# Optimization experiments

Hardware: AMD Instinct MI355X
Metric: run time of the kernel (lower is better)

## Reference

```python
import jax, jax.numpy as jnp
import numpy as np

D_MODEL = 768
D_STATE = 16
D_CONV = 4
EXPAND = 2
HEADDIM = 64
D_INNER = EXPAND * D_MODEL          # 1536
NHEADS = D_INNER // HEADDIM         # 24
CONV_DIM = D_INNER + 2 * D_STATE    # 1568
D_IN_PROJ = 2 * D_INNER + 2 * D_STATE + NHEADS  # 3128
BATCH, SEQ = 4, 2048


def _mamba_params(key, scale=0.02):
    ks = jax.random.split(key, 5)
    return dict(
        in_w=jax.random.normal(ks[0], (D_MODEL, D_IN_PROJ), jnp.float32) * scale,
        conv_w=jax.random.normal(ks[1], (CONV_DIM, D_CONV), jnp.float32) * scale,
        conv_b=jnp.zeros((CONV_DIM,), jnp.float32),
        dt_bias=jax.random.normal(ks[2], (NHEADS,), jnp.float32) * 0.1,
        A_log=jnp.log(jax.random.uniform(ks[3], (NHEADS,), jnp.float32, 1.0, 16.0)),
        D=jnp.ones((NHEADS,), jnp.float32),
        norm_w=jnp.ones((D_INNER,), jnp.float32),
        out_w=jax.random.normal(ks[4], (D_INNER, D_MODEL), jnp.float32) * scale,
    )


def setup_inputs() -> dict:
    key = jax.random.key(0)
    kx, kf, kb, k1, k2 = jax.random.split(key, 5)
    f = _mamba_params(kf)
    b = _mamba_params(kb)
    k1a, k1b = jax.random.split(k1)
    inp = {
        'x': jax.random.normal(kx, (BATCH, SEQ, D_MODEL), jnp.float32),
        'ln1_w': jnp.ones((D_MODEL,), jnp.float32), 'ln1_b': jnp.zeros((D_MODEL,), jnp.float32),
        'ln2_w': jnp.ones((D_MODEL,), jnp.float32), 'ln2_b': jnp.zeros((D_MODEL,), jnp.float32),
        'ffn_w1': jax.random.normal(k1a, (2 * D_MODEL, 4 * D_MODEL), jnp.float32) * 0.02,
        'ffn_b1': jnp.zeros((4 * D_MODEL,), jnp.float32),
        'ffn_w2': jax.random.normal(k1b, (4 * D_MODEL, D_MODEL), jnp.float32) * 0.02,
        'ffn_b2': jnp.zeros((D_MODEL,), jnp.float32),
    }
    for name, p in (('f', f), ('b', b)):
        for k, v in p.items():
            inp[name + '_' + k] = v
    return inp


def _layernorm(x, w, b, eps=1e-5):
    m = jnp.mean(x, -1, keepdims=True)
    v = jnp.mean((x - m) ** 2, -1, keepdims=True)
    return (x - m) * jax.lax.rsqrt(v + eps) * w + b


def _mamba2(u, in_w, conv_w, conv_b, dt_bias, A_log, D, norm_w, out_w):
    b, l, _ = u.shape
    zxbcdt = u @ in_w                               # (b,l,d_in_proj)
    z = zxbcdt[..., :D_INNER]
    xBC = zxbcdt[..., D_INNER:D_INNER + CONV_DIM]
    dt = jax.nn.softplus(zxbcdt[..., -NHEADS:] + dt_bias)   # (b,l,h)
    # depthwise causal conv1d (kernel D_CONV) + SiLU
    xpad = jnp.pad(xBC, ((0, 0), (D_CONV - 1, 0), (0, 0)))
    xc = sum(conv_w[:, k] * xpad[:, k:k + l, :] for k in range(D_CONV)) + conv_b
    xc = jax.nn.silu(xc)
    xh = xc[..., :D_INNER].reshape(b, l, NHEADS, HEADDIM)
    Bm = xc[..., D_INNER:D_INNER + D_STATE]          # (b,l,n), ngroups=1
    Cm = xc[..., D_INNER + D_STATE:]                 # (b,l,n)
    A = -jnp.exp(A_log)                              # (h,)
    dA = jnp.exp(dt * A)                             # (b,l,h)

    def step(h, inp):
        dA_t, dt_t, B_t, C_t, x_t = inp              # (b,h),(b,h),(b,n),(b,n),(b,h,p)
        h = h * dA_t[:, :, None, None] + (dt_t[:, :, None] * x_t)[..., None] * B_t[:, None, None, :]
        y = jnp.einsum('bhpn,bn->bhp', h, C_t)
        return h, y

    h0 = jnp.zeros((b, NHEADS, HEADDIM, D_STATE), u.dtype)
    xs = (dA.transpose(1, 0, 2), dt.transpose(1, 0, 2), Bm.transpose(1, 0, 2),
          Cm.transpose(1, 0, 2), xh.transpose(1, 0, 2, 3))
    _, ys = jax.lax.scan(step, h0, xs)               # ys: (l,b,h,p)
    y = ys.transpose(1, 0, 2, 3) + D[None, None, :, None] * xh
    y = y.reshape(b, l, D_INNER)
    # gated RMSNorm: rmsnorm(y * silu(z)) * weight
    yz = y * jax.nn.silu(z)
    yz = yz * jax.lax.rsqrt(jnp.mean(yz * yz, -1, keepdims=True) + 1e-5) * norm_w
    return yz @ out_w


def reference(x, ln1_w, ln1_b, ln2_w, ln2_b,
              f_in_w, f_conv_w, f_conv_b, f_dt_bias, f_A_log, f_D, f_norm_w, f_out_w,
              b_in_w, b_conv_w, b_conv_b, b_dt_bias, b_A_log, b_D, b_norm_w, b_out_w,
              ffn_w1, ffn_b1, ffn_w2, ffn_b2):
    xn = _layernorm(x, ln1_w, ln1_b)
    fo = _mamba2(xn, f_in_w, f_conv_w, f_conv_b, f_dt_bias, f_A_log, f_D, f_norm_w, f_out_w)
    bo = _mamba2(jnp.flip(xn, 1), b_in_w, b_conv_w, b_conv_b, b_dt_bias, b_A_log, b_D, b_norm_w, b_out_w)
    bo = jnp.flip(bo, 1)
    bi = jnp.concatenate([fo, bo], -1)
    h = jax.nn.gelu(bi @ ffn_w1 + ffn_b1, approximate=False)
    h = jax.nn.gelu(h @ ffn_w2 + ffn_b2, approximate=False)
    # dropout is identity in eval mode
    return _layernorm(x + h, ln2_w, ln2_b)
```

## Files before the change

kernel.cpp:

```cpp
#include <hip/hip_runtime.h>
#include <math.h>

#define BATCH   4
#define SEQ     2048
#define DMODEL  768
#define DSTATE  16
#define DCONV   4
#define HEADDIM 64
#define DINNER  1536
#define NHEADS  24
#define CONVDIM 1568
#define DINPROJ 3128
#define DFFN    3072
#define ROWS    (BATCH*SEQ)
#define QCH     128
#define NCHUNK  (SEQ/QCH)

typedef __attribute__((ext_vector_type(8))) short bhalf8;
typedef __attribute__((ext_vector_type(4))) float floatx4;

__device__ __forceinline__ float gelu_f(float x) {
    return 0.5f * x * (1.0f + erff(x * 0.70710678118654752f));
}

__device__ __forceinline__ void splitRNE(float v, unsigned short& h, unsigned short& l) {
    unsigned u = __float_as_uint(v);
    unsigned rr = u + 0x7FFFu + ((u >> 16) & 1u);
    unsigned short hi = (unsigned short)(rr >> 16);
    float rem = v - __uint_as_float(((unsigned)hi) << 16);
    unsigned u2 = __float_as_uint(rem);
    unsigned r2 = u2 + 0x7FFFu + ((u2 >> 16) & 1u);
    h = hi;
    l = (unsigned short)(r2 >> 16);
}

__device__ __forceinline__ void gl16(const unsigned short* g, unsigned short* l) {
    __builtin_amdgcn_global_load_lds(
        (const __attribute__((address_space(1))) void*)g,
        (__attribute__((address_space(3))) void*)l, 16, 0, 0);
}

__device__ __forceinline__ void bar() {
    asm volatile("" ::: "memory");
    __builtin_amdgcn_s_barrier();
    asm volatile("" ::: "memory");
}

__device__ __forceinline__ float2 blockReduce2(float a, float b) {
    #pragma unroll
    for (int o = 32; o > 0; o >>= 1) {
        a += __shfl_down(a, o, 64);
        b += __shfl_down(b, o, 64);
    }
    __shared__ float sa[4], sb[4];
    int w = threadIdx.x >> 6, lane = threadIdx.x & 63;
    if (lane == 0) { sa[w] = a; sb[w] = b; }
    __syncthreads();
    if (threadIdx.x == 0) {
        int nw = blockDim.x >> 6;
        for (int i = 1; i < nw; ++i) { a += sa[i]; b += sb[i]; }
        sa[0] = a; sb[0] = b;
    }
    __syncthreads();
    return make_float2(sa[0], sb[0]);
}

__global__ __launch_bounds__(256) void ln_kernel(
    const float* __restrict__ x, const float* __restrict__ res,
    const float* __restrict__ w, const float* __restrict__ b,
    float* __restrict__ out)
{
    int r = blockIdx.x;
    const float* xr = x + (size_t)r * DMODEL;
    float v[3]; float s = 0.f, ss = 0.f;
    #pragma unroll
    for (int i = 0; i < 3; ++i) {
        int c = threadIdx.x + i * 256;
        float t = xr[c];
        if (res) t += res[(size_t)r * DMODEL + c];
        v[i] = t; s += t; ss += t * t;
    }
    float2 red = blockReduce2(s, ss);
    float mean = red.x * (1.0f / DMODEL);
    float var  = red.y * (1.0f / DMODEL) - mean * mean;
    float inv  = rsqrtf(var + 1e-5f);
    #pragma unroll
    for (int i = 0; i < 3; ++i) {
        int c = threadIdx.x + i * 256;
        out[(size_t)r * DMODEL + c] = (v[i] - mean) * inv * w[c] + b[c];
    }
}

__global__ __launch_bounds__(256) void ln_split_kernel(
    const float* __restrict__ x,
    const float* __restrict__ w, const float* __restrict__ b,
    unsigned short* __restrict__ H, unsigned short* __restrict__ L)
{
    int r = blockIdx.x;
    const float* xr = x + (size_t)r * DMODEL;
    float v[3]; float s = 0.f, ss = 0.f;
    #pragma unroll
    for (int i = 0; i < 3; ++i) {
        int c = threadIdx.x + i * 256;
        float t = xr[c];
        v[i] = t; s += t; ss += t * t;
    }
    float2 red = blockReduce2(s, ss);
    float mean = red.x * (1.0f / DMODEL);
    float var  = red.y * (1.0f / DMODEL) - mean * mean;
    float inv  = rsqrtf(var + 1e-5f);
    #pragma unroll
    for (int i = 0; i < 3; ++i) {
        int c = threadIdx.x + i * 256;
        float o = (v[i] - mean) * inv * w[c] + b[c];
        unsigned short h, l;
        splitRNE(o, h, l);
        H[(size_t)r * DMODEL + c] = h;
        L[(size_t)r * DMODEL + c] = l;
    }
}

__global__ __launch_bounds__(256) void wconv(
    const float* __restrict__ W, unsigned short* __restrict__ TH,
    unsigned short* __restrict__ TL, int K, int N)
{
    __shared__ float t[32][33];
    int tx = threadIdx.x & 31, ty = threadIdx.x >> 5;
    int kb = blockIdx.y * 32, nb = blockIdx.x * 32;
    #pragma unroll
    for (int i = 0; i < 4; ++i) {
        int k = kb + ty + i * 8, n = nb + tx;
        t[ty + i * 8][tx] = (k < K && n < N) ? W[(size_t)k * N + n] : 0.f;
    }
    __syncthreads();
    #pragma unroll
    for (int i = 0; i < 4; ++i) {
        int n = nb + ty + i * 8, k = kb + tx;
        if (n < N && k < K) {
            unsigned short hi, lo;
            splitRNE(t[tx][ty + i * 8], hi, lo);
            TH[(size_t)n * K + k] = hi;
            TL[(size_t)n * K + k] = lo;
        }
    }
}

__global__ __launch_bounds__(256) void gemm3(
    const unsigned short* __restrict__ AHg, const unsigned short* __restrict__ ALg,
    const unsigned short* __restrict__ BHg, const unsigned short* __restrict__ BLg,
    float* __restrict__ C, unsigned short* __restrict__ CHo, unsigned short* __restrict__ CLo,
    const float* __restrict__ bias,
    int M, int N, int K, int ldc, int coloff,
    int revA, int revC, int act)
{
    (void)M;
    __shared__ __align__(16) unsigned short AsH[2][128 * 32], AsL[2][128 * 32];
    __shared__ __align__(16) unsigned short BsH[2][128 * 32], BsL[2][128 * 32];

    const int tid = threadIdx.x;
    const int m0 = blockIdx.y * 128;
    const int n0 = blockIdx.x * 128;

    size_t aoff[2], boff[2];
    int lofs[2];
    #pragma unroll
    for (int q = 0; q < 2; ++q) {
        int row = (tid >> 2) + 64 * q;
        int sd  = (tid & 3) ^ ((row >> 1) & 3);
        int ar = m0 + row;
        if (revA) ar = (ar & ~(SEQ - 1)) + (SEQ - 1 - (ar & (SEQ - 1)));
        aoff[q] = (size_t)ar * K + sd * 8;
        boff[q] = (size_t)(n0 + row) * K + sd * 8;
        lofs[q] = (tid + 256 * q) * 8;
    }

    auto stage = [&](int k0, int b) {
        #pragma unroll
        for (int q = 0; q < 2; ++q) {
            gl16(AHg + aoff[q] + k0, &AsH[b][lofs[q]]);
            gl16(ALg + aoff[q] + k0, &AsL[b][lofs[q]]);
            gl16(BHg + boff[q] + k0, &BsH[b][lofs[q]]);
            gl16(BLg + boff[q] + k0, &BsL[b][lofs[q]]);
        }
    };

    auto frag = [&](const unsigned short* buf, int row, int slot) -> bhalf8 {
        int sp = slot ^ ((row >> 1) & 3);
        return *(const bhalf8*)(buf + row * 32 + sp * 8);
    };

    const int w = tid >> 6, lane = tid & 63;
    const int rw = (w >> 1) * 64, cw = (w & 1) * 64;
    const int lr = lane & 15;
    const int lq = lane >> 4;

    floatx4 acc[4][4];
    const floatx4 fz = {0.f, 0.f, 0.f, 0.f};
    #pragma unroll
    for (int i = 0; i < 4; ++i)
        #pragma unroll
        for (int j = 0; j < 4; ++j) acc[i][j] = fz;

    const int ktiles = K >> 5;
    stage(0, 0);
    asm volatile("s_waitcnt vmcnt(0)" ::: "memory");
    bar();

    for (int kt = 0; kt < ktiles; ++kt) {
        const int cb = kt & 1;
        if (kt + 1 < ktiles) stage((kt + 1) * 32, cb ^ 1);

        const unsigned short* pAH = AsH[cb];
        const unsigned short* pAL = AsL[cb];
        const unsigned short* pBH = BsH[cb];
        const unsigned short* pBL = BsL[cb];
        bhalf8 ah[4], al[4], bh[4], bl[4];
        #pragma unroll
        for (int i = 0; i < 4; ++i) {
            int ra = rw + i * 16 + lr;
            int rb = cw + i * 16 + lr;
            ah[i] = frag(pAH, ra, lq);
            al[i] = frag(pAL, ra, lq);
            bh[i] = frag(pBH, rb, lq);
            bl[i] = frag(pBL, rb, lq);
        }

        __builtin_amdgcn_s_setprio(1);
        #pragma unroll
        for (int i = 0; i < 4; ++i)
            #pragma unroll
            for (int j = 0; j < 4; ++j) {
                acc[i][j] = __builtin_amdgcn_mfma_f32_16x16x32_bf16(ah[i], bh[j], acc[i][j], 0, 0, 0);
                acc[i][j] = __builtin_amdgcn_mfma_f32_16x16x32_bf16(ah[i], bl[j], acc[i][j], 0, 0, 0);
                acc[i][j] = __builtin_amdgcn_mfma_f32_16x16x32_bf16(al[i], bh[j], acc[i][j], 0, 0, 0);
            }
        __builtin_amdgcn_s_setprio(0);

        asm volatile("s_waitcnt vmcnt(0)" ::: "memory");
        bar();
    }

    #pragma unroll
    for (int i = 0; i < 4; ++i) {
        #pragma unroll
        for (int j = 0; j < 4; ++j) {
            int gc = n0 + cw + j * 16 + lr;
            if (gc < N) {
                float bv = bias ? bias[gc] : 0.f;
                #pragma unroll
                for (int rg = 0; rg < 4; ++rg) {
                    int gm = m0 + rw + i * 16 + lq * 4 + rg;
                    if (revC) gm = (gm & ~(SEQ - 1)) + (SEQ - 1 - (gm & (SEQ - 1)));
                    float v = acc[i][j][rg] + bv;
                    if (act) v = gelu_f(v);
                    size_t o = (size_t)gm * ldc + coloff + gc;
                    if (CHo) {
                        unsigned short h, l;
                        splitRNE(v, h, l);
                        CHo[o] = h; CLo[o] = l;
                    } else {
                        C[o] = v;
                    }
                }
            }
        }
    }
}

__global__ __launch_bounds__(256) void conv_kernel(
    const float* __restrict__ zx, const float* __restrict__ cw,
    const float* __restrict__ cb, float* __restrict__ xcv,
    float* __restrict__ bc)
{
    int cg = blockIdx.x * 256 + threadIdx.x;
    if (cg >= CONVDIM / 4) return;
    int c = cg * 4;
    int r = blockIdx.y;
    int t = r & (SEQ - 1);
    int rb = r & ~(SEQ - 1);
    float4 acc = *(const float4*)&cb[c];
    #pragma unroll
    for (int k = 0; k < DCONV; ++k) {
        int tt = t - (DCONV - 1) + k;
        if (tt >= 0) {
            float4 xv = *(const float4*)&zx[(size_t)(rb + tt) * DINPROJ + DINNER + c];
            acc.x += cw[(c + 0) * DCONV + k] * xv.x;
            acc.y += cw[(c + 1) * DCONV + k] * xv.y;
            acc.z += cw[(c + 2) * DCONV + k] * xv.z;
            acc.w += cw[(c + 3) * DCONV + k] * xv.w;
        }
    }
    float4 v;
    v.x = acc.x / (1.0f + expf(-acc.x));
    v.y = acc.y / (1.0f + expf(-acc.y));
    v.z = acc.z / (1.0f + expf(-acc.z));
    v.w = acc.w / (1.0f + expf(-acc.w));
    if (c < DINNER) *(float4*)&xcv[(size_t)r * DINNER + c] = v;
    else            *(float4*)&bc[(size_t)r * 32 + (c - DINNER)] = v;
}

__global__ __launch_bounds__(256) void dt_kernel(
    const float* __restrict__ zx, const float* __restrict__ dt_bias,
    const float* __restrict__ A_log, float* __restrict__ dtda)
{
    int i = blockIdx.x * 256 + threadIdx.x;
    if (i >= ROWS * NHEADS) return;
    int r = i / NHEADS, h = i - r * NHEADS;
    float v = zx[(size_t)r * DINPROJ + (DINPROJ - NHEADS) + h] + dt_bias[h];
    float dt = (v > 20.f) ? v : log1pf(expf(v));
    float A = -expf(A_log[h]);
    float2 o = make_float2(dt, expf(dt * A));
    *(float2*)&dtda[(size_t)r * 48 + 2 * h] = o;
}

__global__ __launch_bounds__(64) void scan_a(
    const float* __restrict__ xcv, const float* __restrict__ bc,
    const float* __restrict__ dtda, const float* __restrict__ Dp,
    float* __restrict__ yout, float* __restrict__ S, float* __restrict__ cd)
{
    int blk = blockIdx.x;
    int bh = blk / NCHUNK, c = blk - bh * NCHUNK;
    int b = bh / NHEADS, h = bh - b * NHEADS;
    int p = threadIdx.x;
    float hs[DSTATE] = {};
    float Dv = Dp[h];
    float cum = 1.f;
    int t0 = c * QCH;
    for (int t = t0; t < t0 + QCH; ++t) {
        size_t r = (size_t)b * SEQ + t;
        float2 dd = *(const float2*)&dtda[r * 48 + 2 * h];
        float dt = dd.x;
        float dA = dd.y;
        float x  = xcv[r * DINNER + h * HEADDIM + p];
        cum *= dA;
        float coef = dt * x;
        const float* bcr = bc + r * 32;
        float y = 0.f;
        #pragma unroll
        for (int n = 0; n < DSTATE; ++n) {
            hs[n] = hs[n] * dA + coef * bcr[n];
            y += hs[n] * bcr[16 + n];
        }
        yout[r * DINPROJ + DINNER + h * HEADDIM + p] = y + Dv * x;
        if (p == 0) cd[r * NHEADS + h] = cum;
    }
    float* Sp = S + (((size_t)bh * NCHUNK + c) * HEADDIM + p) * DSTATE;
    #pragma unroll
    for (int n = 0; n < DSTATE; ++n) Sp[n] = hs[n];
}

__global__ __launch_bounds__(64) void scan_b(
    const float* __restrict__ cd, float* __restrict__ S)
{
    int bh = blockIdx.x;
    int b = bh / NHEADS, h = bh - b * NHEADS;
    int p = threadIdx.x;
    float H[DSTATE] = {};
    for (int c = 0; c < NCHUNK; ++c) {
        float* Sp = S + (((size_t)bh * NCHUNK + c) * HEADDIM + p) * DSTATE;
        float P = cd[((size_t)b * SEQ + c * QCH + QCH - 1) * NHEADS + h];
        float s[DSTATE];
        #pragma unroll
        for (int n = 0; n < DSTATE; ++n) s[n] = Sp[n];
        #pragma unroll
        for (int n = 0; n < DSTATE; ++n) Sp[n] = H[n];
        #pragma unroll
        for (int n = 0; n < DSTATE; ++n) H[n] = P * H[n] + s[n];
    }
}

__global__ __launch_bounds__(64) void scan_c(
    const float* __restrict__ bc, const float* __restrict__ cd,
    const float* __restrict__ S, float* __restrict__ yout)
{
    int blk = blockIdx.x;
    int bh = blk / (NCHUNK - 1), c = blk - bh * (NCHUNK - 1) + 1;
    int b = bh / NHEADS, h = bh - b * NHEADS;
    int p = threadIdx.x;
    const float* Hp = S + (((size_t)bh * NCHUNK + c) * HEADDIM + p) * DSTATE;
    float H[DSTATE];
    #pragma unroll
    for (int n = 0; n < DSTATE; ++n) H[n] = Hp[n];
    int t0 = c * QCH;
    for (int t = t0; t < t0 + QCH; ++t) {
        size_t r = (size_t)b * SEQ + t;
        const float* Cr = bc + r * 32 + 16;
        float dot = 0.f;
        #pragma unroll
        for (int n = 0; n < DSTATE; ++n) dot += H[n] * Cr[n];
        float cum = cd[r * NHEADS + h];
        yout[r * DINPROJ + DINNER + h * HEADDIM + p] += cum * dot;
    }
}

__global__ __launch_bounds__(256) void gnorm_kernel(
    const float* __restrict__ zx, const float* __restrict__ nw,
    unsigned short* __restrict__ H, unsigned short* __restrict__ L)
{
    int r = blockIdx.x;
    const float* zr = zx + (size_t)r * DINPROJ;
    float v[6]; float ss = 0.f;
    #pragma unroll
    for (int i = 0; i < 6; ++i) {
        int c = threadIdx.x + i * 256;
        float z = zr[c];
        float y = zr[DINNER + c];
        float t = y * z / (1.0f + expf(-z));
        v[i] = t; ss += t * t;
    }
    float2 red = blockReduce2(ss, 0.f);
    float sc = rsqrtf(red.x * (1.0f / DINNER) + 1e-5f);
    #pragma unroll
    for (int i = 0; i < 6; ++i) {
        int c = threadIdx.x + i * 256;
        float o = v[i] * sc * nw[c];
        unsigned short h, l;
        splitRNE(o, h, l);
        H[(size_t)r * DINNER + c] = h;
        L[(size_t)r * DINNER + c] = l;
    }
}

extern "C" void kernel_launch(void* const* d_in, const int* in_sizes, int n_in,
                              void* d_out, int out_size, void* d_ws, size_t ws_size,
                              hipStream_t stream)
{
    (void)in_sizes; (void)n_in; (void)out_size; (void)ws_size;
    const float* x     = (const float*)d_in[0];
    const float* ln1w  = (const float*)d_in[1];
    const float* ln1b  = (const float*)d_in[2];
    const float* ln2w  = (const float*)d_in[3];
    const float* ln2b  = (const float*)d_in[4];
    const float* ffnw1 = (const float*)d_in[5];
    const float* ffnb1 = (const float*)d_in[6];
    const float* ffnw2 = (const float*)d_in[7];
    const float* ffnb2 = (const float*)d_in[8];
    const float* p[2][8];
    for (int d = 0; d < 2; ++d)
        for (int i = 0; i < 8; ++i)
            p[d][i] = (const float*)d_in[9 + d * 8 + i];

    float* ws   = (float*)d_ws;
    float* zx   = ws;
    float* bi   = zx + (size_t)ROWS * DINPROJ;
    float* S    = bi + (size_t)ROWS * DINNER;
    float* Wbuf = S  + (size_t)ROWS * DINNER;
    float* bcb  = Wbuf + 2402304;
    float* dtda = bcb + (size_t)ROWS * 32;
    float* Sbuf = Wbuf;
    float* cdbf = Wbuf + (size_t)BATCH * NHEADS * NCHUNK * HEADDIM * DSTATE;

    unsigned short* xnH = (unsigned short*)d_out;
    unsigned short* xnL = xnH + (size_t)ROWS * DMODEL;
    float* xcv = S;
    unsigned short* znH = (unsigned short*)S;
    unsigned short* znL = znH + (size_t)ROWS * DINNER;
    unsigned short* biH = (unsigned short*)bi;
    unsigned short* biL = biH + (size_t)ROWS * DINNER;
    unsigned short* hmH = (unsigned short*)zx;
    unsigned short* hmL = hmH + (size_t)ROWS * DFFN;
    float* ffo = S + 4718592;

    ln_split_kernel<<<ROWS, 256, 0, stream>>>(x, ln1w, ln1b, xnH, xnL);

    for (int d = 0; d < 2; ++d) {
        unsigned short* WH = (unsigned short*)Wbuf;
        unsigned short* WL = WH + (size_t)DINPROJ * DMODEL;
        wconv<<<dim3((DINPROJ + 31) / 32, DMODEL / 32), 256, 0, stream>>>(
            p[d][0], WH, WL, DMODEL, DINPROJ);
        gemm3<<<dim3((DINPROJ + 127) / 128, ROWS / 128), 256, 0, stream>>>(
            xnH, xnL, WH, WL, zx, nullptr, nullptr, nullptr,
            ROWS, DINPROJ, DMODEL, DINPROJ, 0, d, 0, 0);
        conv_kernel<<<dim3(2, ROWS), 256, 0, stream>>>(zx, p[d][1], p[d][2], xcv, bcb);
        dt_kernel<<<(ROWS * NHEADS + 255) / 256, 256, 0, stream>>>(
            zx, p[d][3], p[d][4], dtda);
        scan_a<<<BATCH * NHEADS * NCHUNK, 64, 0, stream>>>(
            xcv, bcb, dtda, p[d][5], zx, Sbuf, cdbf);
        scan_b<<<BATCH * NHEADS, 64, 0, stream>>>(cdbf, Sbuf);
        scan_c<<<BATCH * NHEADS * (NCHUNK - 1), 64, 0, stream>>>(
            bcb, cdbf, Sbuf, zx);
        gnorm_kernel<<<ROWS, 256, 0, stream>>>(zx, p[d][6], znH, znL);
        unsigned short* WL2 = WH + (size_t)DMODEL * DINNER;
        wconv<<<dim3(DMODEL / 32, DINNER / 32), 256, 0, stream>>>(
            p[d][7], WH, WL2, DINNER, DMODEL);
        gemm3<<<dim3(DMODEL / 128, ROWS / 128), 256, 0, stream>>>(
            znH, znL, WH, WL2, nullptr, biH, biL, nullptr,
            ROWS, DMODEL, DINNER, DINNER, d * DMODEL, 0, d, 0);
    }

    {
        unsigned short* WH = (unsigned short*)S;
        unsigned short* WL = WH + (size_t)DFFN * DINNER;
        wconv<<<dim3(DFFN / 32, DINNER / 32), 256, 0, stream>>>(
            ffnw1, WH, WL, DINNER, DFFN);
        gemm3<<<dim3(DFFN / 128, ROWS / 128), 256, 0, stream>>>(
            biH, biL, WH, WL, nullptr, hmH, hmL, ffnb1,
            ROWS, DFFN, DINNER, DFFN, 0, 0, 0, 1);
    }
    {
        unsigned short* WH = (unsigned short*)S;
        unsigned short* WL = WH + (size_t)DMODEL * DFFN;
        wconv<<<dim3(DMODEL / 32, DFFN / 32), 256, 0, stream>>>(
            ffnw2, WH, WL, DFFN, DMODEL);
        gemm3<<<dim3(DMODEL / 128, ROWS / 128), 256, 0, stream>>>(
            hmH, hmL, WH, WL, ffo, nullptr, nullptr, ffnb2,
            ROWS, DMODEL, DFFN, DMODEL, 0, 0, 0, 1);
    }
    ln_kernel<<<ROWS, 256, 0, stream>>>(x, ffo, ln2w, ln2b, (float*)d_out);
}
```

Before: 1.625 ms.

## Overlap next-tile global loads with MFMA and fuse dt computation into conv kernel

The GEMM main loop now issues the next tile's global loads and waits only for the older batch (vmcnt(8)) before a barrier. The wait is no longer a full drain at the end of each iteration, so loads for tile k+1 stay in flight during compute on tile k. The s_setprio hints are removed and an lgkmcnt wait is added before the closing barrier. Separately, the dt/softplus/exp(dt*A) computation is folded into spare threads of the conv kernel, which removes one launch and its separate pass over zx. The vmcnt count assumes exactly 8 outstanding loads per stage, which is fragile if the stage code changes.

```diff
diff --git a/kernel.cpp b/kernel.cpp
--- a/kernel.cpp
+++ b/kernel.cpp
@@ -203,12 +203,15 @@
 
     const int ktiles = K >> 5;
     stage(0, 0);
-    asm volatile("s_waitcnt vmcnt(0)" ::: "memory");
-    bar();
-
     for (int kt = 0; kt < ktiles; ++kt) {
         const int cb = kt & 1;
-        if (kt + 1 < ktiles) stage((kt + 1) * 32, cb ^ 1);
+        if (kt + 1 < ktiles) {
+            stage((kt + 1) * 32, cb ^ 1);
+            asm volatile("s_waitcnt vmcnt(8)" ::: "memory");
+        } else {
+            asm volatile("s_waitcnt vmcnt(0)" ::: "memory");
+        }
+        bar();
 
         const unsigned short* pAH = AsH[cb];
         const unsigned short* pAL = AsL[cb];
@@ -225,7 +228,6 @@
             bl[i] = frag(pBL, rb, lq);
         }
 
-        __builtin_amdgcn_s_setprio(1);
         #pragma unroll
         for (int i = 0; i < 4; ++i)
             #pragma unroll
@@ -234,9 +236,8 @@
                 acc[i][j] = __builtin_amdgcn_mfma_f32_16x16x32_bf16(ah[i], bl[j], acc[i][j], 0, 0, 0);
                 acc[i][j] = __builtin_amdgcn_mfma_f32_16x16x32_bf16(al[i], bh[j], acc[i][j], 0, 0, 0);
             }
-        __builtin_amdgcn_s_setprio(0);
-
-        asm volatile("s_waitcnt vmcnt(0)" ::: "memory");
+
+        asm volatile("s_waitcnt lgkmcnt(0)" ::: "memory");
         bar();
     }
 
@@ -270,47 +271,49 @@
 __global__ __launch_bounds__(256) void conv_kernel(
     const float* __restrict__ zx, const float* __restrict__ cw,
     const float* __restrict__ cb, float* __restrict__ xcv,
-    float* __restrict__ bc)
+    float* __restrict__ bc,
+    const float* __restrict__ dt_bias, const float* __restrict__ A_log,
+    float* __restrict__ dtda)
 {
     int cg = blockIdx.x * 256 + threadIdx.x;
-    if (cg >= CONVDIM / 4) return;
-    int c = cg * 4;
     int r = blockIdx.y;
-    int t = r & (SEQ - 1);
-    int rb = r & ~(SEQ - 1);
-    float4 acc = *(const float4*)&cb[c];
-    #pragma unroll
-    for (int k = 0; k < DCONV; ++k) {
-        int tt = t - (DCONV - 1) + k;
-        if (tt >= 0) {
-            float4 xv = *(const float4*)&zx[(size_t)(rb + tt) * DINPROJ + DINNER + c];
-            acc.x += cw[(c + 0) * DCONV + k] * xv.x;
-            acc.y += cw[(c + 1) * DCONV + k] * xv.y;
-            acc.z += cw[(c + 2) * DCONV + k] * xv.z;
-            acc.w += cw[(c + 3) * DCONV + k] * xv.w;
-        }
-    }
-    float4 v;
-    v.x = acc.x / (1.0f + expf(-acc.x));
-    v.y = acc.y / (1.0f + expf(-acc.y));
-    v.z = acc.z / (1.0f + expf(-acc.z));
-    v.w = acc.w / (1.0f + expf(-acc.w));
-    if (c < DINNER) *(float4*)&xcv[(size_t)r * DINNER + c] = v;
-    else            *(float4*)&bc[(size_t)r * 32 + (c - DINNER)] = v;
-}
-
-__global__ __launch_bounds__(256) void dt_kernel(
-    const float* __restrict__ zx, const float* __restrict__ dt_bias,
-    const float* __restrict__ A_log, float* __restrict__ dtda)
-{
-    int i = blockIdx.x * 256 + threadIdx.x;
-    if (i >= ROWS * NHEADS) return;
-    int r = i / NHEADS, h = i - r * NHEADS;
-    float v = zx[(size_t)r * DINPROJ + (DINPROJ - NHEADS) + h] + dt_bias[h];
-    float dt = (v > 20.f) ? v : log1pf(expf(v));
-    float A = -expf(A_log[h]);
-    float2 o = make_float2(dt, expf(dt * A));
-    *(float2*)&dtda[(size_t)r * 48 + 2 * h] = o;
+    if (cg < CONVDIM / 4) {
+        int c = cg * 4;
+        int t = r & (SEQ - 1);
+        int rb = r & ~(SEQ - 1);
+        float4 acc = *(const float4*)&cb[c];
+        #pragma unroll
+        for (int k = 0; k < DCONV; ++k) {
+            int tt = t - (DCONV - 1) + k;
+            if (tt >= 0) {
+                float4 xv = *(const float4*)&zx[(size_t)(rb + tt) * DINPROJ + DINNER + c];
+                acc.x += cw[(c + 0) * DCONV + k] * xv.x;
+                acc.y += cw[(c + 1) * DCONV + k] * xv.y;
+                acc.z += cw[(c + 2) * DCONV + k] * xv.z;
+                acc.w += cw[(c + 3) * DCONV + k] * xv.w;
+            }
+        }
+        float4 v;
+        v.x = acc.x / (1.0f + expf(-acc.x));
+        v.y = acc.y / (1.0f + expf(-acc.y));
+        v.z = acc.z / (1.0f + expf(-acc.z));
+        v.w = acc.w / (1.0f + expf(-acc.w));
+        if (c < DINNER) *(float4*)&xcv[(size_t)r * DINNER + c] = v;
+        else            *(float4*)&bc[(size_t)r * 32 + (c - DINNER)] = v;
+    } else if (cg >= CONVDIM / 4 && cg < CONVDIM / 4 + NHEADS / 4) {
+        int h0 = (cg - CONVDIM / 4) * 4;
+        float4 zv = *(const float4*)&zx[(size_t)r * DINPROJ + (DINPROJ - NHEADS) + h0];
+        float zz[4] = {zv.x, zv.y, zv.z, zv.w};
+        #pragma unroll
+        for (int j = 0; j < 4; ++j) {
+            int h = h0 + j;
+            float v = zz[j] + dt_bias[h];
+            float dt = (v > 20.f) ? v : log1pf(expf(v));
+            float A = -expf(A_log[h]);
+            float2 o = make_float2(dt, expf(dt * A));
+            *(float2*)&dtda[(size_t)r * 48 + 2 * h] = o;
+        }
+    }
 }
 
 __global__ __launch_bounds__(64) void scan_a(
@@ -471,9 +474,8 @@
         gemm3<<<dim3((DINPROJ + 127) / 128, ROWS / 128), 256, 0, stream>>>(
             xnH, xnL, WH, WL, zx, nullptr, nullptr, nullptr,
             ROWS, DINPROJ, DMODEL, DINPROJ, 0, d, 0, 0);
-        conv_kernel<<<dim3(2, ROWS), 256, 0, stream>>>(zx, p[d][1], p[d][2], xcv, bcb);
-        dt_kernel<<<(ROWS * NHEADS + 255) / 256, 256, 0, stream>>>(
-            zx, p[d][3], p[d][4], dtda);
+        conv_kernel<<<dim3(2, ROWS), 256, 0, stream>>>(
+            zx, p[d][1], p[d][2], xcv, bcb, p[d][3], p[d][4], dtda);
         scan_a<<<BATCH * NHEADS * NCHUNK, 64, 0, stream>>>(
             xcv, bcb, dtda, p[d][5], zx, Sbuf, cdbf);
         scan_b<<<BATCH * NHEADS, 64, 0, stream>>>(cdbf, Sbuf);
```

Measured after the change: 1.619 ms. Within noise of the previous version (-0.4%).
